# Performance work log

Measured on AMD Instinct MI355X. Metric: run time of the kernel, lower is better.

The kernel has to match this reference:

```python
import jax, jax.numpy as jnp
import numpy as np

B, C, H, W = 8, 256, 48, 48
CR = C // 8  # query/key channel dim of the 1x1 conv projections


def setup_inputs() -> dict:
    key = jax.random.key(0)
    ks = jax.random.split(key, 8)
    s = 0.05  # weight scale
    return {
        "feat_map": jax.random.normal(ks[0], (B, C, H, W), dtype=jnp.float32),
        "w1": jax.random.normal(ks[1], (CR, C), dtype=jnp.float32) * s,
        "b1": jax.random.normal(ks[2], (CR,), dtype=jnp.float32) * s,
        "w2": jax.random.normal(ks[3], (CR, C), dtype=jnp.float32) * s,
        "b2": jax.random.normal(ks[4], (CR,), dtype=jnp.float32) * s,
        "w3": jax.random.normal(ks[5], (C, C), dtype=jnp.float32) * s,
        "b3": jax.random.normal(ks[6], (C,), dtype=jnp.float32) * s,
        "gamma": jnp.asarray(0.1, dtype=jnp.float32),  # torch inits to 0; nonzero for a meaningful baseline
    }


def reference(feat_map, w1, b1, w2, b2, w3, b3, gamma):
    b, c, h, w = feat_map.shape
    n = h * w
    x = feat_map.reshape(b, c, n)                     # [B,C,N]
    # 1x1 convs == per-pixel channel matmuls
    q = jnp.einsum('dc,bcn->bnd', w1, x) + b1         # [B,N,C/8]
    k = jnp.einsum('dc,bcn->bdn', w2, x) + b2[None, :, None]  # [B,C/8,N]
    attn = jax.nn.softmax(jnp.einsum('bnd,bdm->bnm', q, k), axis=-1)  # [B,N,N]
    v = jnp.einsum('dc,bcn->bdn', w3, x) + b3[None, :, None]  # [B,C,N]
    # out[b,c,i] = sum_j v[b,c,j] * attn[b,i,j]  (matches bmm(v, attn^T))
    refine = jnp.einsum('bcj,bij->bci', v, attn).reshape(b, c, h, w)
    return gamma * refine + feat_map
```

## Files before the change

### kernel.cpp

```cpp
#include <hip/hip_runtime.h>
#include <stdint.h>

#define NB  8
#define NC  256
#define NCR 32
#define NSP 2304
#define LOG2E 1.44269504088896340736f

typedef __attribute__((ext_vector_type(8))) short short8;
typedef __attribute__((ext_vector_type(4))) float f32x4;
typedef __attribute__((ext_vector_type(4))) unsigned short us4;
typedef __attribute__((ext_vector_type(2))) unsigned int u32x2;

__device__ __forceinline__ unsigned short f2bf(float f) {
  union { float f; unsigned u; } a; a.f = f;
  unsigned r = (a.u + 0x7FFFu + ((a.u >> 16) & 1u)) >> 16;
  return (unsigned short)r;
}

__device__ __forceinline__ float fexp2(float x) {
#if __has_builtin(__builtin_amdgcn_exp2f)
  return __builtin_amdgcn_exp2f(x);
#else
  return __exp2f(x);
#endif
}

__device__ __forceinline__ u32x2 pack4bf(float a, float b, float c, float d) {
  u32x2 r;
#if __has_builtin(__builtin_amdgcn_cvt_pk_bf16_f32)
  typedef __attribute__((ext_vector_type(2))) __bf16 bf2;
  union { bf2 v; unsigned u; } lo, hi;
  lo.v = __builtin_amdgcn_cvt_pk_bf16_f32(a, b);
  hi.v = __builtin_amdgcn_cvt_pk_bf16_f32(c, d);
  r[0] = lo.u; r[1] = hi.u;
#else
  r[0] = (unsigned)f2bf(a) | ((unsigned)f2bf(b) << 16);
  r[1] = (unsigned)f2bf(c) | ((unsigned)f2bf(d) << 16);
#endif
  return r;
}

typedef __attribute__((address_space(1))) const void* gvoidp;
typedef __attribute__((address_space(3))) void* lvoidp;
#define GLOADLDS16(g, l) __builtin_amdgcn_global_load_lds((gvoidp)(g), (lvoidp)(l), 16, 0, 0)

__global__ __launch_bounds__(256) void k_wprep(const float* __restrict__ w1,
    const float* __restrict__ w2, const float* __restrict__ w3,
    unsigned short* __restrict__ WB) {
  const int idx = blockIdx.x * 256 + threadIdx.x;
  const int gid = idx * 4;
  const int row = gid >> 8, col = gid & 255;
  const float* src;
  if (row < 32)       src = w1 + (size_t)row * NC + col;
  else if (row < 64)  src = w2 + (size_t)(row - 32) * NC + col;
  else                src = w3 + (size_t)(row - 64) * NC + col;
  float4 v = *(const float4*)src;
  us4 pk;
  pk[0] = f2bf(v.x); pk[1] = f2bf(v.y); pk[2] = f2bf(v.z); pk[3] = f2bf(v.w);
  *(us4*)(WB + (size_t)row * NC + col) = pk;
}

__global__ __launch_bounds__(256) void k_proj(const float* __restrict__ x,
    const unsigned short* __restrict__ WB, const float* __restrict__ b1,
    const float* __restrict__ b2, const float* __restrict__ b3,
    unsigned short* __restrict__ Q, unsigned short* __restrict__ K,
    unsigned short* __restrict__ V) {
  __shared__ unsigned short xs[32][264];
  const int n0 = blockIdx.x * 32, b = blockIdx.y;
  const int t = threadIdx.x, lane = t & 63, wave = t >> 6;
  const int col = lane & 15, quad = lane >> 4;
  const float* xb = x + (size_t)b * NC * NSP;
#pragma unroll
  for (int p = 0; p < 8; ++p) {
    const int crow = (t >> 3) + p * 32;
    const int n4 = (t & 7) * 4;
    float4 v = *(const float4*)(xb + (size_t)crow * NSP + n0 + n4);
    xs[n4 + 0][crow] = f2bf(v.x);
    xs[n4 + 1][crow] = f2bf(v.y);
    xs[n4 + 2][crow] = f2bf(v.z);
    xs[n4 + 3][crow] = f2bf(v.w);
  }
  __syncthreads();
  const f32x4 zero4 = {0.f, 0.f, 0.f, 0.f};
  f32x4 acc[5][2];
#pragma unroll
  for (int i = 0; i < 5; ++i)
#pragma unroll
    for (int j = 0; j < 2; ++j) acc[i][j] = zero4;

  for (int kc = 0; kc < 8; ++kc) {
    short8 bf[2];
#pragma unroll
    for (int nt = 0; nt < 2; ++nt)
      bf[nt] = *(const short8*)&xs[nt * 16 + col][kc * 32 + quad * 8];
#pragma unroll
    for (int ml = 0; ml < 5; ++ml) {
      const int m0 = (wave * 5 + ml) * 16;
      const short8 af = *(const short8*)(WB + (size_t)(m0 + col) * NC + kc * 32 + quad * 8);
#pragma unroll
      for (int nt = 0; nt < 2; ++nt)
        acc[ml][nt] = __builtin_amdgcn_mfma_f32_16x16x32_bf16(af, bf[nt], acc[ml][nt], 0, 0, 0);
    }
  }
#pragma unroll
  for (int ml = 0; ml < 5; ++ml) {
    const int m0 = (wave * 5 + ml) * 16;
    const float* bias;
    if (m0 < 32)      bias = b1 + m0;
    else if (m0 < 64) bias = b2 + (m0 - 32);
    else              bias = b3 + (m0 - 64);
    float bv[4];
#pragma unroll
    for (int r = 0; r < 4; ++r) bv[r] = bias[quad * 4 + r];
    if (m0 < 64) {
      unsigned short* dst = (m0 < 32) ? Q : K;
      const float scl = (m0 < 32) ? LOG2E : 1.0f;
      const int d0 = (m0 & 31) + quad * 4;
#pragma unroll
      for (int nt = 0; nt < 2; ++nt) {
        const int n = n0 + nt * 16 + col;
        us4 pk;
#pragma unroll
        for (int r = 0; r < 4; ++r) pk[r] = f2bf((acc[ml][nt][r] + bv[r]) * scl);
        *(us4*)(dst + ((size_t)b * NSP + n) * NCR + d0) = pk;
      }
    } else {
      const int cbase = m0 - 64 + quad * 4;
#pragma unroll
      for (int nt = 0; nt < 2; ++nt) {
        const int n = n0 + nt * 16 + col;
#pragma unroll
        for (int r = 0; r < 4; ++r)
          V[((size_t)b * NC + cbase + r) * NSP + n] = f2bf(acc[ml][nt][r] + bv[r]);
      }
    }
  }
}

__global__ __launch_bounds__(192) void k_attn(const unsigned short* __restrict__ Q,
    const unsigned short* __restrict__ K, const unsigned short* __restrict__ V,
    const float* __restrict__ feat, const float* __restrict__ gamma,
    float* __restrict__ out) {
  __shared__ __align__(16) unsigned short smem[19840];
  unsigned short* Vs = smem;
  unsigned short* Ps = smem + 16384;
  const int lin = blockIdx.x;
  const int b = lin & 7;
  const int rest = lin >> 3;
  const int i0 = (rest % 48) * 48;
  const int ch = (rest / 48) * 128;
  const int t = threadIdx.x, lane = t & 63, wave = t >> 6;
  const int col = lane & 15, quad = lane >> 4;
  const int iw = i0 + wave * 16;
  const unsigned short* Qb = Q + (size_t)b * NSP * NCR;
  const unsigned short* Kb = K + (size_t)b * NSP * NCR;
  const unsigned short* Vb = V + (size_t)b * NC * NSP;
  unsigned short* PsW = Ps + wave * 1152;

  const short8 qa = *(const short8*)(Qb + (size_t)(iw + col) * NCR + quad * 8);
  const f32x4 zero4 = {0.f, 0.f, 0.f, 0.f};
  f32x4 acc[8];
#pragma unroll
  for (int ct = 0; ct < 8; ++ct) acc[ct] = zero4;
  float rs = 0.f;
  const int r8 = lane >> 3, pc = lane & 7, jcs = pc ^ r8;

  short8 kb[4];
#pragma unroll
  for (int mt = 0; mt < 4; ++mt)
    kb[mt] = *(const short8*)(Kb + (size_t)(mt * 16 + col) * NCR + quad * 8);
#pragma unroll
  for (int cix = 0; cix < 6; ++cix) {
    const int q = wave * 6 + cix;
    if (q < 16) {
      const unsigned short* g = Vb + (size_t)(ch + q * 8 + r8) * NSP + jcs * 8;
      GLOADLDS16(g, Vs + q * 512);
    }
  }
#pragma unroll
  for (int mt = 0; mt < 4; ++mt) {
    f32x4 s = __builtin_amdgcn_mfma_f32_16x16x32_bf16(kb[mt], qa, zero4, 0, 0, 0);
    const float e0 = fexp2(s[0]), e1 = fexp2(s[1]), e2 = fexp2(s[2]), e3 = fexp2(s[3]);
    rs += (e0 + e1) + (e2 + e3);
    *(u32x2*)(PsW + col * 72 + mt * 16 + quad * 4) = pack4bf(e0, e1, e2, e3);
  }

  for (int kc = 0; kc < 36; ++kc) {
    __syncthreads();
    const int bufc = kc & 1, bufn = bufc ^ 1;
    const int j1 = (kc + 1) * 64;
    const bool more = (kc + 1 < 36);
    if (more) {
#pragma unroll
      for (int mt = 0; mt < 4; ++mt)
        kb[mt] = *(const short8*)(Kb + (size_t)(j1 + mt * 16 + col) * NCR + quad * 8);
#pragma unroll
      for (int cix = 0; cix < 6; ++cix) {
        const int q = wave * 6 + cix;
        if (q < 16) {
          const unsigned short* g = Vb + (size_t)(ch + q * 8 + r8) * NSP + j1 + jcs * 8;
          GLOADLDS16(g, Vs + bufn * 8192 + q * 512);
        }
      }
    }
    const unsigned short* vsc = Vs + bufc * 8192;
    __builtin_amdgcn_s_setprio(1);
#pragma unroll
    for (int kk = 0; kk < 2; ++kk) {
      const short8 pa = *(const short8*)(PsW + col * 72 + kk * 32 + quad * 8);
#pragma unroll
      for (int ct = 0; ct < 8; ++ct) {
        const short8 vbf = *(const short8*)(vsc + (ct * 16 + col) * 64 +
                                            (((kk * 4 + quad) ^ (col & 7)) * 8));
        acc[ct] = __builtin_amdgcn_mfma_f32_16x16x32_bf16(pa, vbf, acc[ct], 0, 0, 0);
      }
    }
    __builtin_amdgcn_s_setprio(0);
    if (more) {
#pragma unroll
      for (int mt = 0; mt < 4; ++mt) {
        f32x4 s = __builtin_amdgcn_mfma_f32_16x16x32_bf16(kb[mt], qa, zero4, 0, 0, 0);
        const float e0 = fexp2(s[0]), e1 = fexp2(s[1]), e2 = fexp2(s[2]), e3 = fexp2(s[3]);
        rs += (e0 + e1) + (e2 + e3);
        *(u32x2*)(PsW + col * 72 + mt * 16 + quad * 4) = pack4bf(e0, e1, e2, e3);
      }
    }
  }

  rs += __shfl_xor(rs, 16, 64);
  rs += __shfl_xor(rs, 32, 64);
  const float g = gamma[0];
  float rinv[4];
#pragma unroll
  for (int r = 0; r < 4; ++r) rinv[r] = g / __shfl(rs, quad * 4 + r, 64);

  const float* fb = feat + (size_t)b * NC * NSP;
  float* ob = out + (size_t)b * NC * NSP;
#pragma unroll
  for (int ct = 0; ct < 8; ++ct) {
    const size_t a0 = (size_t)(ch + ct * 16 + col) * NSP + iw + quad * 4;
    float4 f = *(const float4*)(fb + a0);
    float4 o;
    o.x = acc[ct][0] * rinv[0] + f.x;
    o.y = acc[ct][1] * rinv[1] + f.y;
    o.z = acc[ct][2] * rinv[2] + f.z;
    o.w = acc[ct][3] * rinv[3] + f.w;
    *(float4*)(ob + a0) = o;
  }
}

#define OFF_Q  0UL
#define OFF_K  1179648UL
#define OFF_V  2359296UL
#define OFF_WB 11796480UL

extern "C" void kernel_launch(void* const* d_in, const int* in_sizes, int n_in,
                              void* d_out, int out_size, void* d_ws, size_t ws_size,
                              hipStream_t stream) {
  const float* feat  = (const float*)d_in[0];
  const float* w1    = (const float*)d_in[1];
  const float* b1    = (const float*)d_in[2];
  const float* w2    = (const float*)d_in[3];
  const float* b2    = (const float*)d_in[4];
  const float* w3    = (const float*)d_in[5];
  const float* b3    = (const float*)d_in[6];
  const float* gamma = (const float*)d_in[7];
  float* out = (float*)d_out;
  char* ws = (char*)d_ws;
  unsigned short* Q  = (unsigned short*)(ws + OFF_Q);
  unsigned short* K  = (unsigned short*)(ws + OFF_K);
  unsigned short* V  = (unsigned short*)(ws + OFF_V);
  unsigned short* WB = (unsigned short*)(ws + OFF_WB);

  hipLaunchKernelGGL(k_wprep, dim3(80), dim3(256), 0, stream, w1, w2, w3, WB);
  hipLaunchKernelGGL(k_proj, dim3(72, NB), dim3(256), 0, stream,
                     feat, WB, b1, b2, b3, Q, K, V);
  hipLaunchKernelGGL(k_attn, dim3(768), dim3(192), 0, stream,
                     Q, K, V, feat, gamma, out);
}
```

Baseline: 155.4 us.

## Split projection into bf16 transpose pass and global-load MFMA projection kernel

Adds a separate kernel that converts the input feature map to bf16 and transposes it to pixel-major layout in workspace, followed by a projection kernel that reads MFMA operands straight from global memory instead of staging through LDS. The goal is to drop the strided transposing LDS writes in the old projection kernel and speed up its operand loads. In exchange it adds an extra launch and a full round trip of the transposed activations through memory. The new path runs only when the workspace is large enough, otherwise the old kernel is used.

Result: slower. 164.0 us (+5.6%).

```diff
diff --git a/kernel.cpp b/kernel.cpp
--- a/kernel.cpp
+++ b/kernel.cpp
@@ -59,6 +59,113 @@
   us4 pk;
   pk[0] = f2bf(v.x); pk[1] = f2bf(v.y); pk[2] = f2bf(v.z); pk[3] = f2bf(v.w);
   *(us4*)(WB + (size_t)row * NC + col) = pk;
+}
+
+__global__ __launch_bounds__(256) void k_xt(const float* __restrict__ x,
+    unsigned short* __restrict__ XT) {
+  __shared__ __align__(16) unsigned short xs[32][264];
+  const int tile = blockIdx.x;
+  const int b = tile / 72, n0 = (tile % 72) * 32;
+  const int t = threadIdx.x, lane = t & 63, wave = t >> 6;
+  const float* xb = x + (size_t)b * NC * NSP;
+  const int cgl = lane & 7, n4g = lane >> 3;
+#pragma unroll
+  for (int p = 0; p < 2; ++p) {
+    const int cg = (p * 4 + wave) * 8 + cgl;
+    const float* src = xb + (size_t)(cg * 4) * NSP + n0 + n4g * 4;
+    f32x4 v0 = *(const f32x4*)(src);
+    f32x4 v1 = *(const f32x4*)(src + NSP);
+    f32x4 v2 = *(const f32x4*)(src + 2 * NSP);
+    f32x4 v3 = *(const f32x4*)(src + 3 * NSP);
+#pragma unroll
+    for (int i = 0; i < 4; ++i) {
+      us4 pk;
+      pk[0] = f2bf(v0[i]); pk[1] = f2bf(v1[i]);
+      pk[2] = f2bf(v2[i]); pk[3] = f2bf(v3[i]);
+      *(us4*)&xs[n4g * 4 + i][cg * 4] = pk;
+    }
+  }
+  __syncthreads();
+  const int n = t >> 3;
+#pragma unroll
+  for (int it = 0; it < 4; ++it) {
+    const int chunk = (t & 7) + it * 8;
+    short8 val = *(const short8*)&xs[n][chunk * 8];
+    *(short8*)(XT + ((size_t)b * NSP + n0 + n) * NC + chunk * 8) = val;
+  }
+}
+
+__global__ __launch_bounds__(256) void k_projg(const unsigned short* __restrict__ XT,
+    const unsigned short* __restrict__ WB, const float* __restrict__ b1,
+    const float* __restrict__ b2, const float* __restrict__ b3,
+    unsigned short* __restrict__ Q, unsigned short* __restrict__ K,
+    unsigned short* __restrict__ V) {
+  __shared__ __align__(16) unsigned short Vt[256][40];
+  const int n0 = blockIdx.x * 32, b = blockIdx.y;
+  const int t = threadIdx.x, lane = t & 63, wave = t >> 6;
+  const int col = lane & 15, quad = lane >> 4;
+  const unsigned short* xtb = XT + ((size_t)b * NSP + n0) * NC;
+  const f32x4 zero4 = {0.f, 0.f, 0.f, 0.f};
+  f32x4 acc[5][2];
+#pragma unroll
+  for (int i = 0; i < 5; ++i)
+#pragma unroll
+    for (int j = 0; j < 2; ++j) acc[i][j] = zero4;
+
+  for (int kc = 0; kc < 8; ++kc) {
+    short8 bfr[2];
+#pragma unroll
+    for (int nt = 0; nt < 2; ++nt)
+      bfr[nt] = *(const short8*)(xtb + (size_t)(nt * 16 + col) * NC + kc * 32 + quad * 8);
+#pragma unroll
+    for (int ml = 0; ml < 5; ++ml) {
+      const int m0 = (wave * 5 + ml) * 16;
+      const short8 af = *(const short8*)(WB + (size_t)(m0 + col) * NC + kc * 32 + quad * 8);
+#pragma unroll
+      for (int nt = 0; nt < 2; ++nt)
+        acc[ml][nt] = __builtin_amdgcn_mfma_f32_16x16x32_bf16(af, bfr[nt], acc[ml][nt], 0, 0, 0);
+    }
+  }
+#pragma unroll
+  for (int ml = 0; ml < 5; ++ml) {
+    const int m0 = (wave * 5 + ml) * 16;
+    const float* bias;
+    if (m0 < 32)      bias = b1 + m0;
+    else if (m0 < 64) bias = b2 + (m0 - 32);
+    else              bias = b3 + (m0 - 64);
+    float bv[4];
+#pragma unroll
+    for (int r = 0; r < 4; ++r) bv[r] = bias[quad * 4 + r];
+    if (m0 < 64) {
+      unsigned short* dst = (m0 < 32) ? Q : K;
+      const float scl = (m0 < 32) ? LOG2E : 1.0f;
+      const int d0 = (m0 & 31) + quad * 4;
+#pragma unroll
+      for (int nt = 0; nt < 2; ++nt) {
+        const int n = n0 + nt * 16 + col;
+        us4 pk;
+#pragma unroll
+        for (int r = 0; r < 4; ++r) pk[r] = f2bf((acc[ml][nt][r] + bv[r]) * scl);
+        *(us4*)(dst + ((size_t)b * NSP + n) * NCR + d0) = pk;
+      }
+    } else {
+      const int cbase = m0 - 64 + quad * 4;
+#pragma unroll
+      for (int nt = 0; nt < 2; ++nt) {
+#pragma unroll
+        for (int r = 0; r < 4; ++r)
+          Vt[cbase + r][nt * 16 + col] = f2bf(acc[ml][nt][r] + bv[r]);
+      }
+    }
+  }
+  __syncthreads();
+  const int chunk = t & 3;
+#pragma unroll
+  for (int it = 0; it < 4; ++it) {
+    const int c = (t >> 2) + it * 64;
+    short8 val = *(const short8*)&Vt[c][chunk * 8];
+    *(short8*)(V + ((size_t)b * NC + c) * NSP + n0 + chunk * 8) = val;
+  }
 }
 
 __global__ __launch_bounds__(256) void k_proj(const float* __restrict__ x,
@@ -254,6 +361,8 @@
 #define OFF_K  1179648UL
 #define OFF_V  2359296UL
 #define OFF_WB 11796480UL
+#define OFF_XT 11960320UL
+#define WS_NEED (OFF_XT + 9437184UL)
 
 extern "C" void kernel_launch(void* const* d_in, const int* in_sizes, int n_in,
                               void* d_out, int out_size, void* d_ws, size_t ws_size,
@@ -272,10 +381,17 @@
   unsigned short* K  = (unsigned short*)(ws + OFF_K);
   unsigned short* V  = (unsigned short*)(ws + OFF_V);
   unsigned short* WB = (unsigned short*)(ws + OFF_WB);
+  unsigned short* XT = (unsigned short*)(ws + OFF_XT);
 
   hipLaunchKernelGGL(k_wprep, dim3(80), dim3(256), 0, stream, w1, w2, w3, WB);
-  hipLaunchKernelGGL(k_proj, dim3(72, NB), dim3(256), 0, stream,
-                     feat, WB, b1, b2, b3, Q, K, V);
+  if (ws_size >= WS_NEED) {
+    hipLaunchKernelGGL(k_xt, dim3(576), dim3(256), 0, stream, feat, XT);
+    hipLaunchKernelGGL(k_projg, dim3(72, NB), dim3(256), 0, stream,
+                       XT, WB, b1, b2, b3, Q, K, V);
+  } else {
+    hipLaunchKernelGGL(k_proj, dim3(72, NB), dim3(256), 0, stream,
+                       feat, WB, b1, b2, b3, Q, K, V);
+  }
   hipLaunchKernelGGL(k_attn, dim3(768), dim3(192), 0, stream,
                      Q, K, V, feat, gamma, out);
 }
```
